# Optimization experiments

Hardware: AMD Instinct MI355X
Metric: run time of the kernel (lower is better)

The kernel has to match this reference:

```python
import jax, jax.numpy as jnp
import numpy as np

N, E, T, IN, H, OUT = 100000, 800000, 8, 3, 32, 64


def _lstm_dir(pre, Whh, bhh, reverse):
    # pre: [T, E, 4H] precomputed input contribution (x @ W_ih^T + b_ih)
    Hh = Whh.shape[1]

    def step(carry, xt):
        h, c = carry
        g = xt + h @ Whh.T + bhh  # [E, 4H], pytorch gate order i,f,g,o
        i = jax.nn.sigmoid(g[:, :Hh])
        f = jax.nn.sigmoid(g[:, Hh:2 * Hh])
        gg = jnp.tanh(g[:, 2 * Hh:3 * Hh])
        o = jax.nn.sigmoid(g[:, 3 * Hh:])
        c = f * c + i * gg
        h = o * jnp.tanh(c)
        return (h, c), None

    init = (jnp.zeros((pre.shape[1], Hh), pre.dtype),
            jnp.zeros((pre.shape[1], Hh), pre.dtype))
    (h, c), _ = jax.lax.scan(step, init, pre, reverse=reverse)
    return c  # final cell state [E, H]


def _mlp(x, W1, W2):
    # MLP(num_layers=2, bias=False): lin1 -> relu -> lin2
    return jax.nn.relu(x @ W1.T) @ W2.T


def setup_inputs() -> dict:
    key = jax.random.key(0)
    ks = jax.random.split(key, 18)
    s = 0.1
    inp = {
        "x": jax.random.normal(ks[0], (N, IN), jnp.float32),
        "edge_traj": jax.random.normal(ks[1], (E, T, 6), jnp.float32),
        "w_ih_f": jax.random.normal(ks[2], (4 * H, 6), jnp.float32) * s,
        "w_hh_f": jax.random.normal(ks[3], (4 * H, H), jnp.float32) * s,
        "b_ih_f": jax.random.normal(ks[4], (4 * H,), jnp.float32) * s,
        "b_hh_f": jax.random.normal(ks[5], (4 * H,), jnp.float32) * s,
        "w_ih_b": jax.random.normal(ks[6], (4 * H, 6), jnp.float32) * s,
        "w_hh_b": jax.random.normal(ks[7], (4 * H, H), jnp.float32) * s,
        "b_ih_b": jax.random.normal(ks[8], (4 * H,), jnp.float32) * s,
        "b_hh_b": jax.random.normal(ks[9], (4 * H,), jnp.float32) * s,
        "coor_w1": jax.random.normal(ks[10], (H, IN), jnp.float32) * s,
        "coor_w2": jax.random.normal(ks[11], (H, H), jnp.float32) * s,
        "nn2_w1": jax.random.normal(ks[12], (H, 3 * H), jnp.float32) * s,
        "nn2_w2": jax.random.normal(ks[13], (H, H), jnp.float32) * s,
        "nn_w1": jax.random.normal(ks[14], (H, H), jnp.float32) * s,
        "nn_w2": jax.random.normal(ks[15], (OUT, H), jnp.float32) * s,
        "edge_index": jax.random.randint(ks[16], (2, E), 0, N, dtype=jnp.int32),
    }
    return inp


def reference(x, edge_traj, w_ih_f, w_hh_f, b_ih_f, b_hh_f,
              w_ih_b, w_hh_b, b_ih_b, b_hh_b,
              coor_w1, coor_w2, nn2_w1, nn2_w2, nn_w1, nn_w2, edge_index):
    # bidirectional 1-layer LSTM over edge trajectories; edge attr = c_t.mean(dim=0)
    pre_f = jnp.einsum('etf,gf->teg', edge_traj, w_ih_f) + b_ih_f
    pre_b = jnp.einsum('etf,gf->teg', edge_traj, w_ih_b) + b_ih_b
    c_f = _lstm_dir(pre_f, w_hh_f, b_hh_f, reverse=False)
    c_b = _lstm_dir(pre_b, w_hh_b, b_hh_b, reverse=True)
    traj_encoding = 0.5 * (c_f + c_b)  # [E, H]

    coor = _mlp(x, coor_w1, coor_w2)  # [N, H]

    src, dst = edge_index[0], edge_index[1]  # flow: source_to_target
    # message: nn2(cat[x_i, x_j, edge_attr]) per edge
    msg_in = jnp.concatenate([coor[dst], coor[src], traj_encoding], axis=-1)  # [E, 3H]
    msg = _mlp(msg_in, nn2_w1, nn2_w2)  # [E, H]
    agg = jax.ops.segment_sum(msg, dst, num_segments=N)  # [N, H]

    out = _mlp(agg, nn_w1, nn_w2)  # [N, OUT]; (note: GINEConv.forward skips (1+eps)*x)
    return out.sum(axis=0)  # [OUT]
```

## Files before the change

kernel.cpp:

```cpp
#include <hip/hip_runtime.h>
#include <hip/hip_bf16.h>

typedef __attribute__((ext_vector_type(8))) short    bf16x8;
typedef __attribute__((ext_vector_type(4))) float    f32x4;
typedef __attribute__((ext_vector_type(4))) unsigned u32x4;

#define MTPW 4
#define LOG2E  1.442695041f
#define LOG2E2 2.885390082f
#define MFMA __builtin_amdgcn_mfma_f32_16x16x32_bf16

__device__ __forceinline__ float rcp_(float v){ return __builtin_amdgcn_rcpf(v); }
__device__ __forceinline__ float exp2_(float v){ return __builtin_amdgcn_exp2f(v); }
__device__ __forceinline__ unsigned pk2(float lo, float hi){
    __hip_bfloat162 h = __float22bfloat162_rn(float2{lo, hi});
    return *(unsigned*)&h;
}
__device__ __forceinline__ float lo2f(unsigned u){ return __uint_as_float(u << 16); }
__device__ __forceinline__ float hi2f(unsigned u){ return __uint_as_float(u & 0xFFFF0000u); }

union U4 { bf16x8 v; unsigned u[4]; };

__device__ __forceinline__ bf16x8 ldw8(const float* __restrict__ p){
    const float4 a = *(const float4*)p;
    const float4 b = *(const float4*)(p + 4);
    U4 r;
    r.u[0] = pk2(a.x, a.y); r.u[1] = pk2(a.z, a.w);
    r.u[2] = pk2(b.x, b.y); r.u[3] = pk2(b.z, b.w);
    return r.v;
}
__device__ __forceinline__ bf16x8 ldw8p(const float* __restrict__ rowp, int lq, float s){
    const float4 a = *(const float4*)(rowp + 4*lq);
    const float4 b = *(const float4*)(rowp + 16 + 4*lq);
    U4 r;
    r.u[0] = pk2(a.x*s, a.y*s); r.u[1] = pk2(a.z*s, a.w*s);
    r.u[2] = pk2(b.x*s, b.y*s); r.u[3] = pk2(b.z*s, b.w*s);
    return r.v;
}

#define LDS_RD8(d0,d1,d2,d3,d4,d5,d6,d7,O0,O1,O2,O3,O4,O5,O6,O7)            \
  asm volatile("ds_read_b128 %0, %8 offset:" O0 "\n\t"                      \
               "ds_read_b128 %1, %8 offset:" O1 "\n\t"                      \
               "ds_read_b128 %2, %8 offset:" O2 "\n\t"                      \
               "ds_read_b128 %3, %8 offset:" O3 "\n\t"                      \
               "ds_read_b128 %4, %8 offset:" O4 "\n\t"                      \
               "ds_read_b128 %5, %8 offset:" O5 "\n\t"                      \
               "ds_read_b128 %6, %8 offset:" O6 "\n\t"                      \
               "ds_read_b128 %7, %8 offset:" O7 "\n\t"                      \
               "s_waitcnt lgkmcnt(0)"                                       \
               : "=&v"(d0),"=&v"(d1),"=&v"(d2),"=&v"(d3),                   \
                 "=&v"(d4),"=&v"(d5),"=&v"(d6),"=&v"(d7)                    \
               : "v"(lds_addr))

__device__ __forceinline__ bf16x8 bc8(u32x4 x){ return __builtin_bit_cast(bf16x8, x); }

__device__ __forceinline__ void gates4(const f32x4 ai, const f32x4 af,
                                       const f32x4 ag, const f32x4 ao,
                                       float c[4], float h[4]){
#pragma unroll
    for (int r = 0; r < 4; ++r) {
        const float Ea = exp2_(ai[r]);
        const float Ef = exp2_(af[r]);
        const float Eg = exp2_(ag[r]);
        const float Eo = exp2_(ao[r]);
        const float p  = (Ea + 1.f) * (Eg + 1.f);
        const float f1 = Ef + 1.f;
        const float num = fmaf(c[r], p, (Eg - 1.f) * f1);
        c[r] = num * rcp_(p * f1);
        const float Ec = exp2_(LOG2E2 * c[r]);
        h[r] = (Ec - 1.f) * rcp_((Eo + 1.f) * (Ec + 1.f));
    }
}

__global__ __launch_bounds__(256) void coor_kernel(
    const float* __restrict__ x, const float* __restrict__ w1,
    const float* __restrict__ w2, unsigned short* __restrict__ coorb, int N)
{
    __shared__ float sW1[96];
    __shared__ float sW2[1024];
    const int tid = threadIdx.x;
    if (tid < 96) sW1[tid] = w1[tid];
    for (int i = tid; i < 1024; i += 256) sW2[i] = w2[i];
    __syncthreads();
    int n = blockIdx.x * 256 + tid;
    if (n >= N) return;
    const float x0 = x[n*3+0], x1 = x[n*3+1], x2 = x[n*3+2];
    float h[32];
#pragma unroll
    for (int k = 0; k < 32; ++k)
        h[k] = fmaxf(sW1[k*3+0]*x0 + sW1[k*3+1]*x1 + sW1[k*3+2]*x2, 0.0f);
    union { uint4 q[4]; unsigned u[16]; } st;
#pragma unroll
    for (int p = 0; p < 16; ++p) {
        float a0 = 0.f, a1 = 0.f;
#pragma unroll
        for (int k = 0; k < 32; ++k) {
            a0 += sW2[(2*p)  *32 + k] * h[k];
            a1 += sW2[(2*p+1)*32 + k] * h[k];
        }
        st.u[p] = pk2(a0, a1);
    }
    uint4* cp = (uint4*)(coorb + (size_t)n * 32);
#pragma unroll
    for (int w = 0; w < 4; ++w) cp[w] = st.q[w];
}

template<int DIR>
__global__ __launch_bounds__(256, 2) void lstm_kernel(
    const float* __restrict__ edge_traj,
    const float* __restrict__ w_ih, const float* __restrict__ w_hh,
    const float* __restrict__ b_ih, const float* __restrict__ b_hh,
    unsigned* __restrict__ cbuf, int E)
{
    __shared__ unsigned lds_w[4096];
    const int tid = threadIdx.x;
    for (int i = tid; i < 512; i += 256) {
        const int m = i >> 6, ln = i & 63;
        const int le2 = ln & 15, lq2 = ln >> 4;
        const int row = 16*m + le2;
        const float s = (m == 4 || m == 5) ? LOG2E2 : -LOG2E;
        const float4 a = *(const float4*)(w_hh + row*32 + 4*lq2);
        const float4 b = *(const float4*)(w_hh + row*32 + 16 + 4*lq2);
        unsigned* wp = &lds_w[(size_t)i * 4];
        wp[0] = pk2(a.x*s, a.y*s); wp[1] = pk2(a.z*s, a.w*s);
        wp[2] = pk2(b.x*s, b.y*s); wp[3] = pk2(b.z*s, b.w*s);
        unsigned* xp = &lds_w[(size_t)(512 + i) * 4];
        if (lq2 == 0) {
            const float* p = w_ih + row * 6;
            xp[0] = pk2(p[0]*s, p[1]*s);
            xp[1] = pk2(p[2]*s, p[3]*s);
            xp[2] = pk2(p[4]*s, p[5]*s);
            xp[3] = pk2((b_ih[row] + b_hh[row])*s, 0.f);
        } else {
            xp[0] = 0u; xp[1] = 0u; xp[2] = 0u; xp[3] = 0u;
        }
    }
    __syncthreads();

    const int lane = tid & 63;
    const int wid  = tid >> 6;
    const int le   = lane & 15;
    const int lq   = lane >> 4;
    const bool l0  = (lq == 0);
    const unsigned lds_addr = (unsigned)(size_t)lds_w + (unsigned)lane * 16u;
    const f32x4 Z4 = {0.f, 0.f, 0.f, 0.f};

    const long pr = (long)blockIdx.x * 4 + wid;
    const long e0 = pr * 32;
    if (e0 >= E) return;
    const long eA = e0 + le, eB = e0 + 16 + le;
    const bool vA = eA < E, vB = eB < E;
    const float* xbA = edge_traj + (vA ? eA : (E - 1)) * 48;
    const float* xbB = edge_traj + (vB ? eB : (E - 1)) * 48;

    U4 hfA, hfB;
    hfA.u[0]=hfA.u[1]=hfA.u[2]=hfA.u[3]=0u;
    hfB.u[0]=hfB.u[1]=hfB.u[2]=hfB.u[3]=0u;
    float clA[4]={0,0,0,0}, chA[4]={0,0,0,0};
    float clB[4]={0,0,0,0}, chB[4]={0,0,0,0};

#pragma unroll
    for (int t = 0; t < 8; ++t) {
        const int te = DIR ? (7 - t) : t;
        U4 xfA, xfB;
        {
            const float* xp = xbA + te * 6;
            const float2 a  = *(const float2*)xp;
            const float2 b2 = *(const float2*)(xp + 2);
            const float2 c2 = *(const float2*)(xp + 4);
            xfA.u[0] = l0 ? pk2(a.x, a.y)   : 0u;
            xfA.u[1] = l0 ? pk2(b2.x, b2.y) : 0u;
            xfA.u[2] = l0 ? pk2(c2.x, c2.y) : 0u;
            xfA.u[3] = l0 ? 0x3f80u         : 0u;
        }
        {
            const float* xp = xbB + te * 6;
            const float2 a  = *(const float2*)xp;
            const float2 b2 = *(const float2*)(xp + 2);
            const float2 c2 = *(const float2*)(xp + 4);
            xfB.u[0] = l0 ? pk2(a.x, a.y)   : 0u;
            xfB.u[1] = l0 ? pk2(b2.x, b2.y) : 0u;
            xfB.u[2] = l0 ? pk2(c2.x, c2.y) : 0u;
            xfB.u[3] = l0 ? 0x3f80u         : 0u;
        }

        u32x4 f0,f1,f2,f3,f4,f5,f6,f7;
        LDS_RD8(f0,f1,f2,f3,f4,f5,f6,f7,
                "0","2048","4096","6144","8192","10240","12288","14336");
        f32x4 aiA = MFMA(bc8(f4), xfA.v, Z4, 0,0,0);
        f32x4 afA = MFMA(bc8(f5), xfA.v, Z4, 0,0,0);
        f32x4 agA = MFMA(bc8(f6), xfA.v, Z4, 0,0,0);
        f32x4 aoA = MFMA(bc8(f7), xfA.v, Z4, 0,0,0);
        f32x4 aiB = MFMA(bc8(f4), xfB.v, Z4, 0,0,0);
        f32x4 afB = MFMA(bc8(f5), xfB.v, Z4, 0,0,0);
        f32x4 agB = MFMA(bc8(f6), xfB.v, Z4, 0,0,0);
        f32x4 aoB = MFMA(bc8(f7), xfB.v, Z4, 0,0,0);
        if (t > 0) {
            aiA = MFMA(bc8(f0), hfA.v, aiA, 0,0,0);
            afA = MFMA(bc8(f1), hfA.v, afA, 0,0,0);
            agA = MFMA(bc8(f2), hfA.v, agA, 0,0,0);
            aoA = MFMA(bc8(f3), hfA.v, aoA, 0,0,0);
            aiB = MFMA(bc8(f0), hfB.v, aiB, 0,0,0);
            afB = MFMA(bc8(f1), hfB.v, afB, 0,0,0);
            agB = MFMA(bc8(f2), hfB.v, agB, 0,0,0);
            aoB = MFMA(bc8(f3), hfB.v, aoB, 0,0,0);
        }
        u32x4 g0,g1,g2,g3,g4,g5,g6,g7;
        LDS_RD8(g0,g1,g2,g3,g4,g5,g6,g7,
                "1024","3072","5120","7168","9216","11264","13312","15360");
        float hlA[4], hlB[4];
        gates4(aiA, afA, agA, aoA, clA, hlA);
        gates4(aiB, afB, agB, aoB, clB, hlB);

        f32x4 biA = MFMA(bc8(g4), xfA.v, Z4, 0,0,0);
        f32x4 bfA = MFMA(bc8(g5), xfA.v, Z4, 0,0,0);
        f32x4 bgA = MFMA(bc8(g6), xfA.v, Z4, 0,0,0);
        f32x4 boA = MFMA(bc8(g7), xfA.v, Z4, 0,0,0);
        f32x4 biB = MFMA(bc8(g4), xfB.v, Z4, 0,0,0);
        f32x4 bfB = MFMA(bc8(g5), xfB.v, Z4, 0,0,0);
        f32x4 bgB = MFMA(bc8(g6), xfB.v, Z4, 0,0,0);
        f32x4 boB = MFMA(bc8(g7), xfB.v, Z4, 0,0,0);
        if (t > 0) {
            biA = MFMA(bc8(g0), hfA.v, biA, 0,0,0);
            bfA = MFMA(bc8(g1), hfA.v, bfA, 0,0,0);
            bgA = MFMA(bc8(g2), hfA.v, bgA, 0,0,0);
            boA = MFMA(bc8(g3), hfA.v, boA, 0,0,0);
            biB = MFMA(bc8(g0), hfB.v, biB, 0,0,0);
            bfB = MFMA(bc8(g1), hfB.v, bfB, 0,0,0);
            bgB = MFMA(bc8(g2), hfB.v, bgB, 0,0,0);
            boB = MFMA(bc8(g3), hfB.v, boB, 0,0,0);
        }
        float hhA[4], hhB[4];
        gates4(biA, bfA, bgA, boA, chA, hhA);
        gates4(biB, bfB, bgB, boB, chB, hhB);

        if (t < 7) {
            hfA.u[0] = pk2(hlA[0], hlA[1]); hfA.u[1] = pk2(hlA[2], hlA[3]);
            hfA.u[2] = pk2(hhA[0], hhA[1]); hfA.u[3] = pk2(hhA[2], hhA[3]);
            hfB.u[0] = pk2(hlB[0], hlB[1]); hfB.u[1] = pk2(hlB[2], hlB[3]);
            hfB.u[2] = pk2(hhB[0], hhB[1]); hfB.u[3] = pk2(hhB[2], hhB[3]);
        }
    }

#pragma unroll
    for (int p = 0; p < 2; ++p) {
        const float* cl = p ? clB : clA;
        const float* ch = p ? chB : chA;
        const bool  vst = p ? vB : vA;
        const long  er  = p ? eB : eA;
        if (!vst) continue;
        U4 cw;
        cw.u[0] = pk2(cl[0], cl[1]);
        cw.u[1] = pk2(cl[2], cl[3]);
        cw.u[2] = pk2(ch[0], ch[1]);
        cw.u[3] = pk2(ch[2], ch[3]);
        unsigned* dp = cbuf + er * 16 + lq * 4;
        if (DIR == 0) {
            *(uint4*)dp = *(uint4*)cw.u;
        } else {
            const uint4 f = *(const uint4*)dp;
            uint4 o;
            o.x = pk2(0.5f*(lo2f(f.x)+lo2f(cw.u[0])), 0.5f*(hi2f(f.x)+hi2f(cw.u[0])));
            o.y = pk2(0.5f*(lo2f(f.y)+lo2f(cw.u[1])), 0.5f*(hi2f(f.y)+hi2f(cw.u[1])));
            o.z = pk2(0.5f*(lo2f(f.z)+lo2f(cw.u[2])), 0.5f*(hi2f(f.z)+hi2f(cw.u[2])));
            o.w = pk2(0.5f*(lo2f(f.w)+lo2f(cw.u[3])), 0.5f*(hi2f(f.w)+hi2f(cw.u[3])));
            *(uint4*)dp = o;
        }
    }
}

__global__ __launch_bounds__(256, 4) void msg_kernel(
    unsigned* trmsg,
    const float* __restrict__ nn2_w1, const float* __restrict__ nn2_w2,
    const int* __restrict__ edge_index,
    const unsigned short* __restrict__ coorb, int E)
{
    const int lane = threadIdx.x & 63;
    const int wid  = threadIdx.x >> 6;
    const int le   = lane & 15;
    const int lq   = lane >> 4;
    const f32x4 Z4 = {0.f, 0.f, 0.f, 0.f};

    bf16x8 w1a[2][3], w2a[2];
#pragma unroll
    for (int mm = 0; mm < 2; ++mm) {
        const int row = 16*mm + le;
        w1a[mm][0] = ldw8(nn2_w1 + row*96 +  8*lq);
        w1a[mm][1] = ldw8(nn2_w1 + row*96 + 32 + 8*lq);
        w1a[mm][2] = ldw8p(nn2_w1 + row*96 + 64, lq, 1.0f);
        w2a[mm]    = ldw8p(nn2_w2 + row*32, lq, 1.0f);
    }

    const long gw = (long)blockIdx.x * 4 + wid;
    for (int it = 0; it < MTPW; ++it) {
        const long tile = gw * MTPW + it;
        const long e0 = tile * 16;
        if (e0 >= E) break;
        const long e_raw = e0 + le;
        const bool valid = e_raw < E;
        const long ec = valid ? e_raw : (E - 1);

        U4 tf;
        if (valid) *(uint4*)tf.u = *(const uint4*)(trmsg + e_raw * 16 + lq * 4);
        else tf.u[0] = tf.u[1] = tf.u[2] = tf.u[3] = 0u;

        const int src = edge_index[ec];
        const int dst = edge_index[E + ec];
        U4 df, sf;
        {
            const uint4 dv = *(const uint4*)(coorb + (size_t)dst*32 + lq*8);
            const uint4 sv = *(const uint4*)(coorb + (size_t)src*32 + lq*8);
            df.u[0]=dv.x; df.u[1]=dv.y; df.u[2]=dv.z; df.u[3]=dv.w;
            sf.u[0]=sv.x; sf.u[1]=sv.y; sf.u[2]=sv.z; sf.u[3]=sv.w;
        }

        f32x4 h1[2];
#pragma unroll
        for (int mm = 0; mm < 2; ++mm) {
            f32x4 a = MFMA(w1a[mm][0], df.v, Z4, 0,0,0);
            a = MFMA(w1a[mm][1], sf.v, a, 0,0,0);
            a = MFMA(w1a[mm][2], tf.v, a, 0,0,0);
            h1[mm] = a;
        }
        U4 gf;
        gf.u[0] = pk2(fmaxf(h1[0][0],0.f), fmaxf(h1[0][1],0.f));
        gf.u[1] = pk2(fmaxf(h1[0][2],0.f), fmaxf(h1[0][3],0.f));
        gf.u[2] = pk2(fmaxf(h1[1][0],0.f), fmaxf(h1[1][1],0.f));
        gf.u[3] = pk2(fmaxf(h1[1][2],0.f), fmaxf(h1[1][3],0.f));

        const f32x4 o0 = MFMA(w2a[0], gf.v, Z4, 0,0,0);
        const f32x4 o1 = MFMA(w2a[1], gf.v, Z4, 0,0,0);
        if (valid) {
            U4 cw;
            cw.u[0] = pk2(o0[0], o0[1]);
            cw.u[1] = pk2(o0[2], o0[3]);
            cw.u[2] = pk2(o1[0], o1[1]);
            cw.u[3] = pk2(o1[2], o1[3]);
            *(uint4*)(trmsg + e_raw * 16 + lq * 4) = *(uint4*)cw.u;
        }
    }
}

__global__ __launch_bounds__(256) void hist_kernel(
    const int* __restrict__ ei, int* __restrict__ cnt, int E)
{
    const int e = blockIdx.x*256 + threadIdx.x;
    if (e < E) atomicAdd(&cnt[ei[E + e]], 1);
}

__global__ __launch_bounds__(256) void scan1_kernel(
    const int* __restrict__ cnt, int* __restrict__ bsum, int N)
{
    __shared__ int sp[4];
    const int tid = threadIdx.x;
    const int n = blockIdx.x*256 + tid;
    int c = (n < N) ? cnt[n] : 0;
#pragma unroll
    for (int m = 1; m < 64; m <<= 1) c += __shfl_xor(c, m, 64);
    if ((tid & 63) == 0) sp[tid >> 6] = c;
    __syncthreads();
    if (tid == 0) bsum[blockIdx.x] = sp[0] + sp[1] + sp[2] + sp[3];
}

__global__ __launch_bounds__(512) void scan2_kernel(
    int* __restrict__ bsum, int* __restrict__ offs, int nblk, int E, int N)
{
    __shared__ int s[512];
    const int tid = threadIdx.x;
    const int v = (tid < nblk) ? bsum[tid] : 0;
    s[tid] = v;
    __syncthreads();
    for (int off = 1; off < 512; off <<= 1) {
        const int t = (tid >= off) ? s[tid - off] : 0;
        __syncthreads();
        s[tid] += t;
        __syncthreads();
    }
    if (tid < nblk) bsum[tid] = s[tid] - v;
    if (tid == 0) offs[N] = E;
}

__global__ __launch_bounds__(256) void scan3_kernel(
    const int* __restrict__ cnt, const int* __restrict__ bsum,
    int* __restrict__ offs, int* __restrict__ cursor, int N)
{
    __shared__ int s[256];
    const int tid = threadIdx.x;
    const int n = blockIdx.x*256 + tid;
    const int v = (n < N) ? cnt[n] : 0;
    s[tid] = v;
    __syncthreads();
    for (int off = 1; off < 256; off <<= 1) {
        const int t = (tid >= off) ? s[tid - off] : 0;
        __syncthreads();
        s[tid] += t;
        __syncthreads();
    }
    if (n < N) {
        const int o = bsum[blockIdx.x] + s[tid] - v;
        offs[n] = o;
        cursor[n] = o;
    }
}

__global__ __launch_bounds__(256) void fill_kernel(
    const int* __restrict__ ei, int* __restrict__ cursor,
    int* __restrict__ eidx, int E)
{
    const int e = blockIdx.x*256 + threadIdx.x;
    if (e < E) {
        const int p = atomicAdd(&cursor[ei[E + e]], 1);
        eidx[p] = e;
    }
}

__global__ __launch_bounds__(256) void gather_kernel(
    const unsigned* __restrict__ msg, const int* __restrict__ offs,
    const int* __restrict__ eidx, float* __restrict__ aggv, int N)
{
    const int lane = threadIdx.x & 63;
    const int wid  = threadIdx.x >> 6;
    const int g  = lane >> 4;
    const int le = lane & 15;
    const int n = blockIdx.x*16 + wid*4 + g;
    if (n >= N) return;
    const int beg = offs[n], end = offs[n+1];
    float sx = 0.f, sy = 0.f;
    for (int i = beg; i < end; ++i) {
        const unsigned w = msg[(size_t)eidx[i]*16 + le];
        sx += lo2f(w); sy += hi2f(w);
    }
    *(float2*)(aggv + (size_t)n*32 + 2*le) = float2{sx, sy};
}

__global__ __launch_bounds__(256) void agg_kernel(
    const float* __restrict__ aggv, const float* __restrict__ nn_w1,
    float* __restrict__ partials, int N)
{
    __shared__ float sW[1024];
    __shared__ float sP[4][32];
    const int tid = threadIdx.x;
    for (int i = tid; i < 1024; i += 256) {
        const int jj = i >> 5, s = i & 31, q = s >> 3, j = s & 7;
        const int col = (j < 4) ? (4*q + j) : (16 + 4*q + (j - 4));
        sW[i] = nn_w1[jj*32 + col];
    }
    __syncthreads();
    const int n = blockIdx.x*256 + tid;
    float h[32];
    if (n < N) {
        float a[32];
        const float4* ap = (const float4*)(aggv + (size_t)n*32);
#pragma unroll
        for (int k4 = 0; k4 < 8; ++k4) {
            const float4 v = ap[k4];
            a[k4*4]=v.x; a[k4*4+1]=v.y; a[k4*4+2]=v.z; a[k4*4+3]=v.w;
        }
#pragma unroll
        for (int jj = 0; jj < 32; ++jj) {
            float acc = 0.f;
#pragma unroll
            for (int k = 0; k < 32; ++k) acc += sW[jj*32+k]*a[k];
            h[jj] = fmaxf(acc, 0.f);
        }
    } else {
#pragma unroll
        for (int jj = 0; jj < 32; ++jj) h[jj] = 0.f;
    }
#pragma unroll
    for (int m = 1; m < 64; m <<= 1) {
#pragma unroll
        for (int k = 0; k < 32; ++k) h[k] += __shfl_xor(h[k], m, 64);
    }
    if ((tid & 63) == 0) {
#pragma unroll
        for (int k = 0; k < 32; ++k) sP[tid >> 6][k] = h[k];
    }
    __syncthreads();
    if (tid < 32)
        partials[(size_t)blockIdx.x * 32 + tid]
            = sP[0][tid] + sP[1][tid] + sP[2][tid] + sP[3][tid];
}

__global__ __launch_bounds__(256) void reduce_kernel(
    const float* __restrict__ partials, const float* __restrict__ nn_w2,
    float* __restrict__ out, int nblk)
{
    __shared__ float sR[8][32];
    __shared__ float sS[32];
    const int tid = threadIdx.x;
    const int col = tid & 31;
    const int row = tid >> 5;
    float s = 0.f;
    for (int i = row; i < nblk; i += 8) s += partials[(size_t)i*32 + col];
    sR[row][col] = s;
    __syncthreads();
    if (row == 0) {
        float t = 0.f;
#pragma unroll
        for (int r = 0; r < 8; ++r) t += sR[r][col];
        sS[col] = t;
    }
    __syncthreads();
    if (tid < 64) {
        float acc = 0.f;
#pragma unroll
        for (int k = 0; k < 32; ++k) acc += nn_w2[tid*32+k] * sS[k];
        out[tid] = acc;
    }
}

extern "C" void kernel_launch(void* const* d_in, const int* in_sizes, int n_in,
                              void* d_out, int out_size, void* d_ws, size_t ws_size,
                              hipStream_t stream)
{
    const float* x         = (const float*)d_in[0];
    const float* edge_traj = (const float*)d_in[1];
    const float* w_ih_f    = (const float*)d_in[2];
    const float* w_hh_f    = (const float*)d_in[3];
    const float* b_ih_f    = (const float*)d_in[4];
    const float* b_hh_f    = (const float*)d_in[5];
    const float* w_ih_b    = (const float*)d_in[6];
    const float* w_hh_b    = (const float*)d_in[7];
    const float* b_ih_b    = (const float*)d_in[8];
    const float* b_hh_b    = (const float*)d_in[9];
    const float* coor_w1   = (const float*)d_in[10];
    const float* coor_w2   = (const float*)d_in[11];
    const float* nn2_w1    = (const float*)d_in[12];
    const float* nn2_w2    = (const float*)d_in[13];
    const float* nn_w1     = (const float*)d_in[14];
    const float* nn_w2     = (const float*)d_in[15];
    const int* edge_index  = (const int*)d_in[16];
    const int N = in_sizes[0] / 3;
    const int E = in_sizes[16] / 2;
    const int nblk = (N + 255) / 256;

    float* aggv = (float*)d_ws;
    float* partials = aggv + (size_t)N * 32;
    unsigned short* coorb = (unsigned short*)(partials + (size_t)nblk * 32);
    unsigned* cbuf = (unsigned*)(coorb + (size_t)N * 32);
    int* cnt    = (int*)(cbuf + (size_t)E * 16);
    int* offs   = cnt + N;
    int* cursor = offs + N + 1;
    int* eidx   = cursor + N;
    int* bsum   = eidx + E;

    (void)hipMemsetAsync(cnt, 0, (size_t)N * sizeof(int), stream);

    coor_kernel<<<nblk, 256, 0, stream>>>(x, coor_w1, coor_w2, coorb, N);

    const long tiles   = ((long)E + 15) / 16;
    const long pairs   = (tiles + 1) / 2;
    const int  lblocks = (int)((pairs + 3) / 4);
    lstm_kernel<0><<<lblocks, 256, 0, stream>>>(edge_traj,
        w_ih_f, w_hh_f, b_ih_f, b_hh_f, cbuf, E);
    lstm_kernel<1><<<lblocks, 256, 0, stream>>>(edge_traj,
        w_ih_b, w_hh_b, b_ih_b, b_hh_b, cbuf, E);

    const int eblk = (E + 255) / 256;
    hist_kernel<<<eblk, 256, 0, stream>>>(edge_index, cnt, E);
    scan1_kernel<<<nblk, 256, 0, stream>>>(cnt, bsum, N);
    scan2_kernel<<<1, 512, 0, stream>>>(bsum, offs, nblk, E, N);
    scan3_kernel<<<nblk, 256, 0, stream>>>(cnt, bsum, offs, cursor, N);
    fill_kernel<<<eblk, 256, 0, stream>>>(edge_index, cursor, eidx, E);

    const int mblocks = (int)((tiles + 4*MTPW - 1) / (4*MTPW));
    msg_kernel<<<mblocks, 256, 0, stream>>>(cbuf, nn2_w1, nn2_w2,
        edge_index, coorb, E);

    gather_kernel<<<(N + 15)/16, 256, 0, stream>>>(cbuf, offs, eidx, aggv, N);
    agg_kernel<<<nblk, 256, 0, stream>>>(aggv, nn_w1, partials, N);
    reduce_kernel<<<1, 256, 0, stream>>>(partials, nn_w2, (float*)d_out, nblk);
}
```

Measured before the change: 653.3 us.

## Process one edge tile per wave in LSTM and skip dead gate work

Each LSTM wave now processes a single 16-edge tile instead of two, and launch bounds go from 2 to 4 blocks per SM to raise occupancy. It also specializes the first and last timesteps. At t=0 the forget gate is skipped because the cell state is zero, and at t=7 the output gate and h are skipped because only c is used. This removes some MFMA and transcendental work. The trade-off is less per-wave instruction-level parallelism and twice as many blocks, so the LDS weight setup is repeated more often.

```diff
diff --git a/kernel.cpp b/kernel.cpp
--- a/kernel.cpp
+++ b/kernel.cpp
@@ -54,9 +54,21 @@
 
 __device__ __forceinline__ bf16x8 bc8(u32x4 x){ return __builtin_bit_cast(bf16x8, x); }
 
-__device__ __forceinline__ void gates4(const f32x4 ai, const f32x4 af,
-                                       const f32x4 ag, const f32x4 ao,
-                                       float c[4], float h[4]){
+__device__ __forceinline__ void gates4_first(const f32x4 ai, const f32x4 ag, const f32x4 ao,
+                                             float c[4], float h[4]){
+#pragma unroll
+    for (int r = 0; r < 4; ++r) {
+        const float Ea = exp2_(ai[r]);
+        const float Eg = exp2_(ag[r]);
+        const float Eo = exp2_(ao[r]);
+        c[r] = (Eg - 1.f) * rcp_((Ea + 1.f) * (Eg + 1.f));
+        const float Ec = exp2_(LOG2E2 * c[r]);
+        h[r] = (Ec - 1.f) * rcp_((Eo + 1.f) * (Ec + 1.f));
+    }
+}
+__device__ __forceinline__ void gates4_mid(const f32x4 ai, const f32x4 af,
+                                           const f32x4 ag, const f32x4 ao,
+                                           float c[4], float h[4]){
 #pragma unroll
     for (int r = 0; r < 4; ++r) {
         const float Ea = exp2_(ai[r]);
@@ -71,6 +83,19 @@
         h[r] = (Ec - 1.f) * rcp_((Eo + 1.f) * (Ec + 1.f));
     }
 }
+__device__ __forceinline__ void gates4_last(const f32x4 ai, const f32x4 af,
+                                            const f32x4 ag, float c[4]){
+#pragma unroll
+    for (int r = 0; r < 4; ++r) {
+        const float Ea = exp2_(ai[r]);
+        const float Ef = exp2_(af[r]);
+        const float Eg = exp2_(ag[r]);
+        const float p  = (Ea + 1.f) * (Eg + 1.f);
+        const float f1 = Ef + 1.f;
+        const float num = fmaf(c[r], p, (Eg - 1.f) * f1);
+        c[r] = num * rcp_(p * f1);
+    }
+}
 
 __global__ __launch_bounds__(256) void coor_kernel(
     const float* __restrict__ x, const float* __restrict__ w1,
@@ -106,7 +131,7 @@
 }
 
 template<int DIR>
-__global__ __launch_bounds__(256, 2) void lstm_kernel(
+__global__ __launch_bounds__(256, 4) void lstm_kernel(
     const float* __restrict__ edge_traj,
     const float* __restrict__ w_ih, const float* __restrict__ w_hh,
     const float* __restrict__ b_ih, const float* __restrict__ b_hh,
@@ -145,110 +170,76 @@
     const unsigned lds_addr = (unsigned)(size_t)lds_w + (unsigned)lane * 16u;
     const f32x4 Z4 = {0.f, 0.f, 0.f, 0.f};
 
-    const long pr = (long)blockIdx.x * 4 + wid;
-    const long e0 = pr * 32;
+    const long tile = (long)blockIdx.x * 4 + wid;
+    const long e0 = tile * 16;
     if (e0 >= E) return;
-    const long eA = e0 + le, eB = e0 + 16 + le;
-    const bool vA = eA < E, vB = eB < E;
-    const float* xbA = edge_traj + (vA ? eA : (E - 1)) * 48;
-    const float* xbB = edge_traj + (vB ? eB : (E - 1)) * 48;
-
-    U4 hfA, hfB;
-    hfA.u[0]=hfA.u[1]=hfA.u[2]=hfA.u[3]=0u;
-    hfB.u[0]=hfB.u[1]=hfB.u[2]=hfB.u[3]=0u;
-    float clA[4]={0,0,0,0}, chA[4]={0,0,0,0};
-    float clB[4]={0,0,0,0}, chB[4]={0,0,0,0};
+    const long er = e0 + le;
+    const bool valid = er < E;
+    const float* xb = edge_traj + (valid ? er : (E - 1)) * 48;
+
+    U4 hf; hf.u[0]=hf.u[1]=hf.u[2]=hf.u[3]=0u;
+    float cl[4]={0,0,0,0}, ch[4]={0,0,0,0};
 
 #pragma unroll
     for (int t = 0; t < 8; ++t) {
         const int te = DIR ? (7 - t) : t;
-        U4 xfA, xfB;
+        U4 xf;
         {
-            const float* xp = xbA + te * 6;
+            const float* xp = xb + te * 6;
             const float2 a  = *(const float2*)xp;
             const float2 b2 = *(const float2*)(xp + 2);
             const float2 c2 = *(const float2*)(xp + 4);
-            xfA.u[0] = l0 ? pk2(a.x, a.y)   : 0u;
-            xfA.u[1] = l0 ? pk2(b2.x, b2.y) : 0u;
-            xfA.u[2] = l0 ? pk2(c2.x, c2.y) : 0u;
-            xfA.u[3] = l0 ? 0x3f80u         : 0u;
-        }
-        {
-            const float* xp = xbB + te * 6;
-            const float2 a  = *(const float2*)xp;
-            const float2 b2 = *(const float2*)(xp + 2);
-            const float2 c2 = *(const float2*)(xp + 4);
-            xfB.u[0] = l0 ? pk2(a.x, a.y)   : 0u;
-            xfB.u[1] = l0 ? pk2(b2.x, b2.y) : 0u;
-            xfB.u[2] = l0 ? pk2(c2.x, c2.y) : 0u;
-            xfB.u[3] = l0 ? 0x3f80u         : 0u;
+            xf.u[0] = l0 ? pk2(a.x, a.y)   : 0u;
+            xf.u[1] = l0 ? pk2(b2.x, b2.y) : 0u;
+            xf.u[2] = l0 ? pk2(c2.x, c2.y) : 0u;
+            xf.u[3] = l0 ? 0x3f80u         : 0u;
         }
 
         u32x4 f0,f1,f2,f3,f4,f5,f6,f7;
         LDS_RD8(f0,f1,f2,f3,f4,f5,f6,f7,
                 "0","2048","4096","6144","8192","10240","12288","14336");
-        f32x4 aiA = MFMA(bc8(f4), xfA.v, Z4, 0,0,0);
-        f32x4 afA = MFMA(bc8(f5), xfA.v, Z4, 0,0,0);
-        f32x4 agA = MFMA(bc8(f6), xfA.v, Z4, 0,0,0);
-        f32x4 aoA = MFMA(bc8(f7), xfA.v, Z4, 0,0,0);
-        f32x4 aiB = MFMA(bc8(f4), xfB.v, Z4, 0,0,0);
-        f32x4 afB = MFMA(bc8(f5), xfB.v, Z4, 0,0,0);
-        f32x4 agB = MFMA(bc8(f6), xfB.v, Z4, 0,0,0);
-        f32x4 aoB = MFMA(bc8(f7), xfB.v, Z4, 0,0,0);
+        f32x4 ai = MFMA(bc8(f4), xf.v, Z4, 0,0,0);
+        f32x4 af = Z4, ao = Z4;
+        if (t != 0) af = MFMA(bc8(f5), xf.v, Z4, 0,0,0);
+        f32x4 ag = MFMA(bc8(f6), xf.v, Z4, 0,0,0);
+        if (t != 7) ao = MFMA(bc8(f7), xf.v, Z4, 0,0,0);
         if (t > 0) {
-            aiA = MFMA(bc8(f0), hfA.v, aiA, 0,0,0);
-            afA = MFMA(bc8(f1), hfA.v, afA, 0,0,0);
-            agA = MFMA(bc8(f2), hfA.v, agA, 0,0,0);
-            aoA = MFMA(bc8(f3), hfA.v, aoA, 0,0,0);
-            aiB = MFMA(bc8(f0), hfB.v, aiB, 0,0,0);
-            afB = MFMA(bc8(f1), hfB.v, afB, 0,0,0);
-            agB = MFMA(bc8(f2), hfB.v, agB, 0,0,0);
-            aoB = MFMA(bc8(f3), hfB.v, aoB, 0,0,0);
+            ai = MFMA(bc8(f0), hf.v, ai, 0,0,0);
+            af = MFMA(bc8(f1), hf.v, af, 0,0,0);
+            ag = MFMA(bc8(f2), hf.v, ag, 0,0,0);
+            if (t != 7) ao = MFMA(bc8(f3), hf.v, ao, 0,0,0);
         }
         u32x4 g0,g1,g2,g3,g4,g5,g6,g7;
         LDS_RD8(g0,g1,g2,g3,g4,g5,g6,g7,
                 "1024","3072","5120","7168","9216","11264","13312","15360");
-        float hlA[4], hlB[4];
-        gates4(aiA, afA, agA, aoA, clA, hlA);
-        gates4(aiB, afB, agB, aoB, clB, hlB);
-
-        f32x4 biA = MFMA(bc8(g4), xfA.v, Z4, 0,0,0);
-        f32x4 bfA = MFMA(bc8(g5), xfA.v, Z4, 0,0,0);
-        f32x4 bgA = MFMA(bc8(g6), xfA.v, Z4, 0,0,0);
-        f32x4 boA = MFMA(bc8(g7), xfA.v, Z4, 0,0,0);
-        f32x4 biB = MFMA(bc8(g4), xfB.v, Z4, 0,0,0);
-        f32x4 bfB = MFMA(bc8(g5), xfB.v, Z4, 0,0,0);
-        f32x4 bgB = MFMA(bc8(g6), xfB.v, Z4, 0,0,0);
-        f32x4 boB = MFMA(bc8(g7), xfB.v, Z4, 0,0,0);
+
+        float hl[4], hh[4];
+        if (t == 0)      gates4_first(ai, ag, ao, cl, hl);
+        else if (t == 7) gates4_last(ai, af, ag, cl);
+        else             gates4_mid(ai, af, ag, ao, cl, hl);
+
+        f32x4 bi = MFMA(bc8(g4), xf.v, Z4, 0,0,0);
+        f32x4 bf = Z4, bo = Z4;
+        if (t != 0) bf = MFMA(bc8(g5), xf.v, Z4, 0,0,0);
+        f32x4 bg = MFMA(bc8(g6), xf.v, Z4, 0,0,0);
+        if (t != 7) bo = MFMA(bc8(g7), xf.v, Z4, 0,0,0);
         if (t > 0) {
-            biA = MFMA(bc8(g0), hfA.v, biA, 0,0,0);
-            bfA = MFMA(bc8(g1), hfA.v, bfA, 0,0,0);
-            bgA = MFMA(bc8(g2), hfA.v, bgA, 0,0,0);
-            boA = MFMA(bc8(g3), hfA.v, boA, 0,0,0);
-            biB = MFMA(bc8(g0), hfB.v, biB, 0,0,0);
-            bfB = MFMA(bc8(g1), hfB.v, bfB, 0,0,0);
-            bgB = MFMA(bc8(g2), hfB.v, bgB, 0,0,0);
-            boB = MFMA(bc8(g3), hfB.v, boB, 0,0,0);
-        }
-        float hhA[4], hhB[4];
-        gates4(biA, bfA, bgA, boA, chA, hhA);
-        gates4(biB, bfB, bgB, boB, chB, hhB);
+            bi = MFMA(bc8(g0), hf.v, bi, 0,0,0);
+            bf = MFMA(bc8(g1), hf.v, bf, 0,0,0);
+            bg = MFMA(bc8(g2), hf.v, bg, 0,0,0);
+            if (t != 7) bo = MFMA(bc8(g3), hf.v, bo, 0,0,0);
+        }
+        if (t == 0)      gates4_first(bi, bg, bo, ch, hh);
+        else if (t == 7) gates4_last(bi, bf, bg, ch);
+        else             gates4_mid(bi, bf, bg, bo, ch, hh);
 
         if (t < 7) {
-            hfA.u[0] = pk2(hlA[0], hlA[1]); hfA.u[1] = pk2(hlA[2], hlA[3]);
-            hfA.u[2] = pk2(hhA[0], hhA[1]); hfA.u[3] = pk2(hhA[2], hhA[3]);
-            hfB.u[0] = pk2(hlB[0], hlB[1]); hfB.u[1] = pk2(hlB[2], hlB[3]);
-            hfB.u[2] = pk2(hhB[0], hhB[1]); hfB.u[3] = pk2(hhB[2], hhB[3]);
-        }
-    }
-
-#pragma unroll
-    for (int p = 0; p < 2; ++p) {
-        const float* cl = p ? clB : clA;
-        const float* ch = p ? chB : chA;
-        const bool  vst = p ? vB : vA;
-        const long  er  = p ? eB : eA;
-        if (!vst) continue;
+            hf.u[0] = pk2(hl[0], hl[1]); hf.u[1] = pk2(hl[2], hl[3]);
+            hf.u[2] = pk2(hh[0], hh[1]); hf.u[3] = pk2(hh[2], hh[3]);
+        }
+    }
+
+    if (valid) {
         U4 cw;
         cw.u[0] = pk2(cl[0], cl[1]);
         cw.u[1] = pk2(cl[2], cl[3]);
@@ -550,8 +541,7 @@
     coor_kernel<<<nblk, 256, 0, stream>>>(x, coor_w1, coor_w2, coorb, N);
 
     const long tiles   = ((long)E + 15) / 16;
-    const long pairs   = (tiles + 1) / 2;
-    const int  lblocks = (int)((pairs + 3) / 4);
+    const int  lblocks = (int)((tiles + 3) / 4);
     lstm_kernel<0><<<lblocks, 256, 0, stream>>>(edge_traj,
         w_ih_f, w_hh_f, b_ih_f, b_hh_f, cbuf, E);
     lstm_kernel<1><<<lblocks, 256, 0, stream>>>(edge_traj,
```

Result: faster. 607.0 us (-7.1%).
